# Kernel optimization log

Measured on AMD Instinct MI355X. Metric: run time of the kernel, lower is better.

The kernel has to match this reference:

```python
import jax, jax.numpy as jnp
import numpy as np

B, D, H, N, M, S = 64, 256, 512, 16384, 64, 3
EPS = 1e-4


def setup_inputs() -> dict:
    key = jax.random.key(0)
    ks = jax.random.split(key, 20)
    rn = lambda k, shape, sc=1.0: jax.random.normal(k, shape, dtype=jnp.float32) * sc
    z = lambda n: jnp.zeros((n,), jnp.float32)
    sc = 0.05
    return {
        "inp": rn(ks[0], (B, D)),
        "h_tm1": rn(ks[1], (B, H), 0.1),
        "c_tm1": rn(ks[2], (B, H), 0.1),
        "read_tm1": jax.nn.softmax(rn(ks[3], (B, N)), axis=-1),
        "write_tm1": jax.nn.softmax(rn(ks[4], (B, N)), axis=-1),
        "memory": rn(ks[5], (B, N, M), 0.1),
        "W_ih": rn(ks[6], (4 * H, D + M), sc), "b_ih": z(4 * H),
        "W_hh": rn(ks[7], (4 * H, H), sc), "b_hh": z(4 * H),
        "W_rk": rn(ks[8], (M, H), sc), "b_rk": z(M),
        "W_wk": rn(ks[9], (M, H), sc), "b_wk": z(M),
        "W_rc": rn(ks[10], (3, H), sc), "b_rc": z(3),
        "W_wc": rn(ks[11], (3, H), sc), "b_wc": z(3),
        "W_rs": rn(ks[12], (S, H), sc), "b_rs": z(S),
        "W_ws": rn(ks[13], (S, H), sc), "b_ws": z(S),
        "W_w": rn(ks[14], (2 * M, H), sc), "b_w": z(2 * M),
    }


def _head_params(h, Wk, bk, Wc, bc, Ws, bs):
    k = jnp.tanh(h @ Wk.T + bk)                 # [B, M] key
    c = h @ Wc.T + bc                           # [B, 3] beta/g/gamma raw
    s = jax.nn.softmax(h @ Ws.T + bs, axis=-1)  # [B, S] shift dist
    beta = jax.nn.relu(c[:, 0:1]) + EPS
    g = jax.nn.sigmoid(c[:, 1:2])
    gamma = jax.nn.relu(c[:, 2:3]) + 1.0 + EPS
    return k, s, beta, g, gamma


def _address(memory, w_tm1, k, s, beta, g, gamma):
    # content addressing: beta-scaled cosine similarity, softmax over slots
    dot = jnp.einsum('bm,bnm->bn', k, memory)                    # [B, N]
    nM = jnp.sqrt(jnp.sum(memory * memory, axis=-1)) + EPS       # [B, N]
    nk = jnp.sqrt(jnp.sum(k * k, axis=-1, keepdims=True)) + EPS  # [B, 1]
    content = jax.nn.softmax(beta * dot / (nM * nk), axis=-1)
    # interpolation with previous head
    inter = g * content + (1.0 - g) * w_tm1                      # [B, N]
    # circular shift conv: out[j] = sum_r s[r] * inter[(j + r - (S-1)) mod N]
    shifted = jnp.stack([jnp.roll(inter, S - 1 - r, axis=1) for r in range(S)], axis=-1)  # [B, N, S]
    conv = jnp.einsum('bns,bs->bn', shifted, s)
    # sharpening
    sharp = jnp.maximum(conv, 1e-8) ** gamma
    return sharp / jnp.sum(sharp, axis=1, keepdims=True)


def reference(inp, h_tm1, c_tm1, read_tm1, write_tm1, memory,
              W_ih, b_ih, W_hh, b_hh, W_rk, b_rk, W_wk, b_wk,
              W_rc, b_rc, W_wc, b_wc, W_rs, b_rs, W_ws, b_ws, W_w, b_w):
    # read head addressed from previous hidden state
    rk, rs, rbeta, rg, rgamma = _head_params(h_tm1, W_rk, b_rk, W_rc, b_rc, W_rs, b_rs)
    read_head = _address(memory, read_tm1, rk, rs, rbeta, rg, rgamma)
    M_read = jnp.einsum('bn,bnm->bm', read_head, memory)         # [B, M]
    # LSTMCell controller (torch gate order i, f, g, o)
    x = jnp.concatenate([inp, M_read], axis=1)
    gates = x @ W_ih.T + b_ih + h_tm1 @ W_hh.T + b_hh
    i, f, gg, o = jnp.split(gates, 4, axis=1)
    c_t = jax.nn.sigmoid(f) * c_tm1 + jax.nn.sigmoid(i) * jnp.tanh(gg)
    h_t = jax.nn.sigmoid(o) * jnp.tanh(c_t)
    # write head addressed from new hidden state
    wk, ws, wbeta, wg, wgamma = _head_params(h_t, W_wk, b_wk, W_wc, b_wc, W_ws, b_ws)
    write_head = _address(memory, write_tm1, wk, ws, wbeta, wg, wgamma)
    wa = h_t @ W_w.T + b_w
    e = jax.nn.sigmoid(wa[:, :M])                                # erase [B, M]
    a = wa[:, M:]                                                # add   [B, M]
    ww = write_head[:, :, None]                                  # [B, N, 1]
    M_out = memory * (1.0 - ww * e[:, None, :]) + ww * a[:, None, :]
    return (h_t, c_t, read_head, write_head, M_out)
```

## Files before the change

### kernel.cpp

```cpp
#include <hip/hip_runtime.h>
#include <hip/hip_bf16.h>
#include <math.h>

#define B_  64
#define D_  256
#define H_  512
#define N_  16384
#define M_  64
#define S_  3
#define EPS_ 1e-4f

__device__ __forceinline__ float sigmoidf_(float x) { return 1.0f / (1.0f + expf(-x)); }

template <bool WITH_W>
__global__ __launch_bounds__(256) void head_params_kernel(
    const float* __restrict__ h,
    const float* __restrict__ Wk, const float* __restrict__ bk,
    const float* __restrict__ Wc, const float* __restrict__ bc,
    const float* __restrict__ Ws, const float* __restrict__ bs,
    const float* __restrict__ Ww, const float* __restrict__ bw,
    float* __restrict__ k_out, float* __restrict__ nk_out,
    float* __restrict__ s_out,
    float* __restrict__ beta_out, float* __restrict__ g_out, float* __restrict__ gamma_out,
    float* __restrict__ e_out, float* __restrict__ a_out)
{
    const int b = blockIdx.x;
    const int tid = threadIdx.x;
    const int lane = tid & 63;
    const int wid = tid >> 6;
    __shared__ float raw[198];

    float h8[8];
    #pragma unroll
    for (int j = 0; j < 8; ++j) h8[j] = h[b * H_ + lane + 64 * j];

    const int count = WITH_W ? 198 : 70;
    for (int r = wid; r < count; r += 4) {
        const float* wrow;
        float bias;
        if (r < 64)       { wrow = Wk + r * H_;        bias = bk[r]; }
        else if (r < 67)  { wrow = Wc + (r - 64) * H_; bias = bc[r - 64]; }
        else if (r < 70)  { wrow = Ws + (r - 67) * H_; bias = bs[r - 67]; }
        else              { wrow = Ww + (r - 70) * H_; bias = bw[r - 70]; }
        float acc = 0.f;
        #pragma unroll
        for (int j = 0; j < 8; ++j) acc += wrow[lane + 64 * j] * h8[j];
        for (int off = 32; off >= 1; off >>= 1) acc += __shfl_xor(acc, off);
        if (lane == 0) raw[r] = acc + bias;
    }
    __syncthreads();

    if (tid < 64) {
        float kv = tanhf(raw[tid]);
        k_out[b * 64 + tid] = kv;
        float sq = kv * kv;
        for (int off = 32; off >= 1; off >>= 1) sq += __shfl_xor(sq, off);
        if (tid == 0) nk_out[b] = sqrtf(sq) + EPS_;
    } else if (tid == 64) {
        float c0 = raw[64], c1 = raw[65], c2 = raw[66];
        beta_out[b]  = fmaxf(c0, 0.f) + EPS_;
        g_out[b]     = sigmoidf_(c1);
        gamma_out[b] = fmaxf(c2, 0.f) + 1.f + EPS_;
    } else if (tid == 65) {
        float s0 = raw[67], s1 = raw[68], s2 = raw[69];
        float mx = fmaxf(s0, fmaxf(s1, s2));
        float e0 = expf(s0 - mx), e1 = expf(s1 - mx), e2 = expf(s2 - mx);
        float inv = 1.f / (e0 + e1 + e2);
        s_out[b * 3 + 0] = e0 * inv;
        s_out[b * 3 + 1] = e1 * inv;
        s_out[b * 3 + 2] = e2 * inv;
    }
    if (WITH_W && tid >= 128 && tid < 192) {
        int m = tid - 128;
        e_out[b * 64 + m] = sigmoidf_(raw[70 + m]);
        a_out[b * 64 + m] = raw[134 + m];
    }
}

template <bool COMPUTE_NM>
__global__ __launch_bounds__(256) void dot_kernel(
    const float* __restrict__ memory,
    const float* __restrict__ k,
    float* __restrict__ dot,
    float* __restrict__ nM)
{
    const int tid = threadIdx.x;
    const int lane = tid & 63;
    const int wid = tid >> 6;
    const int grp = lane >> 4;
    const int m16 = lane & 15;
    const int b = blockIdx.x >> 8;
    const int nbase = (blockIdx.x & 255) * 64;
    const float4 k4 = ((const float4*)(k + b * 64))[m16];
    const int slot = wid * 4 + grp;
    const size_t bbase = (size_t)b * N_;
    #pragma unroll
    for (int it = 0; it < 4; ++it) {
        const int n = nbase + it * 16 + slot;
        const float4 m4 = ((const float4*)(memory + (bbase + n) * 64))[m16];
        float d  = m4.x * k4.x + m4.y * k4.y + m4.z * k4.z + m4.w * k4.w;
        float sq = m4.x * m4.x + m4.y * m4.y + m4.z * m4.z + m4.w * m4.w;
        for (int off = 8; off >= 1; off >>= 1) {
            d += __shfl_xor(d, off);
            if (COMPUTE_NM) sq += __shfl_xor(sq, off);
        }
        if (m16 == 0) {
            dot[bbase + n] = d;
            if (COMPUTE_NM) nM[bbase + n] = sqrtf(sq) + EPS_;
        }
    }
}

__global__ __launch_bounds__(1024) void address_kernel(
    const float* __restrict__ dot,
    const float* __restrict__ nM,
    const float* __restrict__ w_tm1,
    const float* __restrict__ nk_a,
    const float* __restrict__ beta_a, const float* __restrict__ g_a,
    const float* __restrict__ gamma_a, const float* __restrict__ s_a,
    float* __restrict__ head_out)
{
    __shared__ float lds[N_];
    const int tid = threadIdx.x;
    const int b = blockIdx.x;
    const size_t base = (size_t)b * N_;
    const float beta = beta_a[b], g = g_a[b], gamma = gamma_a[b], nk = nk_a[b];
    const float s0 = s_a[b * 3 + 0], s1 = s_a[b * 3 + 1], s2 = s_a[b * 3 + 2];

    float lg[16];
    float lmax = -1e30f;
    #pragma unroll
    for (int t = 0; t < 16; ++t) {
        const int n = t * 1024 + tid;
        const float x = beta * dot[base + n] / (nM[base + n] * nk);
        lg[t] = x;
        lmax = fmaxf(lmax, x);
    }
    for (int off = 32; off >= 1; off >>= 1) lmax = fmaxf(lmax, __shfl_xor(lmax, off));
    if ((tid & 63) == 0) lds[tid >> 6] = lmax;
    __syncthreads();
    if (tid == 0) {
        float v = lds[0];
        for (int i = 1; i < 16; ++i) v = fmaxf(v, lds[i]);
        lds[16] = v;
    }
    __syncthreads();
    const float gmax = lds[16];

    float lsum = 0.f;
    #pragma unroll
    for (int t = 0; t < 16; ++t) { lg[t] = expf(lg[t] - gmax); lsum += lg[t]; }
    for (int off = 32; off >= 1; off >>= 1) lsum += __shfl_xor(lsum, off);
    if ((tid & 63) == 0) lds[tid >> 6] = lsum;
    __syncthreads();
    if (tid == 0) {
        float v = 0.f;
        for (int i = 0; i < 16; ++i) v += lds[i];
        lds[16] = v;
    }
    __syncthreads();
    const float inv_sum = 1.f / lds[16];
    __syncthreads();

    #pragma unroll
    for (int t = 0; t < 16; ++t) {
        const int n = t * 1024 + tid;
        lds[n] = g * lg[t] * inv_sum + (1.f - g) * w_tm1[base + n];
    }
    __syncthreads();

    float sh[16];
    float lsum2 = 0.f;
    #pragma unroll
    for (int t = 0; t < 16; ++t) {
        const int n = t * 1024 + tid;
        const float conv = s2 * lds[n] + s1 * lds[(n + N_ - 1) & (N_ - 1)]
                         + s0 * lds[(n + N_ - 2) & (N_ - 1)];
        const float v = powf(fmaxf(conv, 1e-8f), gamma);
        sh[t] = v;
        lsum2 += v;
    }
    __syncthreads();
    for (int off = 32; off >= 1; off >>= 1) lsum2 += __shfl_xor(lsum2, off);
    if ((tid & 63) == 0) lds[tid >> 6] = lsum2;
    __syncthreads();
    if (tid == 0) {
        float v = 0.f;
        for (int i = 0; i < 16; ++i) v += lds[i];
        lds[16] = v;
    }
    __syncthreads();
    const float inv2 = 1.f / lds[16];
    #pragma unroll
    for (int t = 0; t < 16; ++t) head_out[base + t * 1024 + tid] = sh[t] * inv2;
}

__global__ __launch_bounds__(256) void m_read_kernel(
    const float* __restrict__ memory,
    const float* __restrict__ head,
    float* __restrict__ M_read)
{
    const int tid = threadIdx.x;
    const int lane = tid & 63;
    const int wid = tid >> 6;
    const int grp = lane >> 4;
    const int m16 = lane & 15;
    const int b = blockIdx.x >> 6;
    const int nbase = (blockIdx.x & 63) * 256;
    const int slot = wid * 4 + grp;
    const size_t bbase = (size_t)b * N_;
    float4 acc = make_float4(0.f, 0.f, 0.f, 0.f);
    #pragma unroll 4
    for (int it = 0; it < 16; ++it) {
        const int n = nbase + it * 16 + slot;
        const float w = head[bbase + n];
        const float4 m4 = ((const float4*)(memory + (bbase + n) * 64))[m16];
        acc.x += w * m4.x; acc.y += w * m4.y; acc.z += w * m4.z; acc.w += w * m4.w;
    }
    for (int off = 32; off >= 16; off >>= 1) {
        acc.x += __shfl_xor(acc.x, off);
        acc.y += __shfl_xor(acc.y, off);
        acc.z += __shfl_xor(acc.z, off);
        acc.w += __shfl_xor(acc.w, off);
    }
    __shared__ float4 part[64];
    if (lane < 16) part[wid * 16 + lane] = acc;
    __syncthreads();
    if (tid < 16) {
        float4 t = part[tid];
        for (int w = 1; w < 4; ++w) {
            const float4 p = part[w * 16 + tid];
            t.x += p.x; t.y += p.y; t.z += p.z; t.w += p.w;
        }
        atomicAdd(&M_read[b * 64 + tid * 4 + 0], t.x);
        atomicAdd(&M_read[b * 64 + tid * 4 + 1], t.y);
        atomicAdd(&M_read[b * 64 + tid * 4 + 2], t.z);
        atomicAdd(&M_read[b * 64 + tid * 4 + 3], t.w);
    }
}

__global__ __launch_bounds__(256) void gates_splitk_kernel(
    const float* __restrict__ inp,
    const float* __restrict__ M_read,
    const float* __restrict__ h_tm1,
    const float* __restrict__ W_ih,
    const float* __restrict__ W_hh,
    float* __restrict__ gates)
{
    __shared__ __align__(16) float Xsm[64][68];
    __shared__ __align__(16) float Wsm[64][68];
    const int tid = threadIdx.x;
    const int jb = blockIdx.x & 31;
    const int c  = blockIdx.x >> 5;
    const int j0 = jb * 64;

    #pragma unroll
    for (int i = 0; i < 4; ++i) {
        const int e = i * 256 + tid;
        const int row = e >> 4;
        const int c4 = e & 15;
        const float* xrow;
        if (c < 4)       xrow = inp    + row * 256 + c * 64;
        else if (c == 4) xrow = M_read + row * 64;
        else             xrow = h_tm1  + row * 512 + (c - 5) * 64;
        const float4 v = ((const float4*)xrow)[c4];
        const int kl = c4 * 4;
        Xsm[kl + 0][row] = v.x; Xsm[kl + 1][row] = v.y;
        Xsm[kl + 2][row] = v.z; Xsm[kl + 3][row] = v.w;
    }
    #pragma unroll
    for (int i = 0; i < 4; ++i) {
        const int e = i * 256 + tid;
        const int row = e >> 4;
        const int c4 = e & 15;
        const float* wrow;
        if (c < 5) wrow = W_ih + (j0 + row) * 320 + c * 64;
        else       wrow = W_hh + (j0 + row) * 512 + (c - 5) * 64;
        const float4 v = ((const float4*)wrow)[c4];
        const int kl = c4 * 4;
        Wsm[kl + 0][row] = v.x; Wsm[kl + 1][row] = v.y;
        Wsm[kl + 2][row] = v.z; Wsm[kl + 3][row] = v.w;
    }
    __syncthreads();

    const int tx = tid & 15, ty = tid >> 4;
    float acc[4][4] = {};
    #pragma unroll
    for (int k = 0; k < 64; ++k) {
        const float4 av = *((const float4*)&Xsm[k][ty * 4]);
        const float4 wv = *((const float4*)&Wsm[k][tx * 4]);
        acc[0][0] += av.x * wv.x; acc[0][1] += av.x * wv.y; acc[0][2] += av.x * wv.z; acc[0][3] += av.x * wv.w;
        acc[1][0] += av.y * wv.x; acc[1][1] += av.y * wv.y; acc[1][2] += av.y * wv.z; acc[1][3] += av.y * wv.w;
        acc[2][0] += av.z * wv.x; acc[2][1] += av.z * wv.y; acc[2][2] += av.z * wv.z; acc[2][3] += av.z * wv.w;
        acc[3][0] += av.w * wv.x; acc[3][1] += av.w * wv.y; acc[3][2] += av.w * wv.z; acc[3][3] += av.w * wv.w;
    }
    #pragma unroll
    for (int bi = 0; bi < 4; ++bi) {
        const int b = ty * 4 + bi;
        #pragma unroll
        for (int ji = 0; ji < 4; ++ji) {
            atomicAdd(&gates[b * 2048 + j0 + tx * 4 + ji], acc[bi][ji]);
        }
    }
}

__global__ __launch_bounds__(256) void lstm_kernel(
    const float* __restrict__ gates,
    const float* __restrict__ b_ih, const float* __restrict__ b_hh,
    const float* __restrict__ c_tm1,
    float* __restrict__ h_out, float* __restrict__ c_out)
{
    const int idx = blockIdx.x * 256 + threadIdx.x;
    const int b = idx >> 9, j = idx & 511;
    const float* gr = gates + b * 2048;
    const float i_ = sigmoidf_(gr[j]        + b_ih[j]        + b_hh[j]);
    const float f_ = sigmoidf_(gr[512 + j]  + b_ih[512 + j]  + b_hh[512 + j]);
    const float g_ = tanhf(   gr[1024 + j] + b_ih[1024 + j] + b_hh[1024 + j]);
    const float o_ = sigmoidf_(gr[1536 + j] + b_ih[1536 + j] + b_hh[1536 + j]);
    const float c = f_ * c_tm1[idx] + i_ * g_;
    c_out[idx] = c;
    h_out[idx] = o_ * tanhf(c);
}

__global__ __launch_bounds__(256) void m_out_kernel(
    const float* __restrict__ memory,
    const float* __restrict__ whead,
    const float* __restrict__ e,
    const float* __restrict__ a,
    float* __restrict__ M_out)
{
    const size_t total = (size_t)B_ * N_ * 16;
    const size_t stride = (size_t)gridDim.x * 256;
    for (size_t idx = (size_t)blockIdx.x * 256 + threadIdx.x; idx < total; idx += stride) {
        const size_t nlin = idx >> 4;
        const int m4 = (int)(idx & 15);
        const int b = (int)(nlin >> 14);
        const float w = whead[nlin];
        const float4 ev = ((const float4*)(e + b * 64))[m4];
        const float4 av = ((const float4*)(a + b * 64))[m4];
        const float4 mv = ((const float4*)memory)[idx];
        float4 o;
        o.x = mv.x * (1.f - w * ev.x) + w * av.x;
        o.y = mv.y * (1.f - w * ev.y) + w * av.y;
        o.z = mv.z * (1.f - w * ev.z) + w * av.z;
        o.w = mv.w * (1.f - w * ev.w) + w * av.w;
        ((float4*)M_out)[idx] = o;
    }
}

extern "C" void kernel_launch(void* const* d_in, const int* in_sizes, int n_in,
                              void* d_out, int out_size, void* d_ws, size_t ws_size,
                              hipStream_t stream)
{
    const float* inp       = (const float*)d_in[0];
    const float* h_tm1     = (const float*)d_in[1];
    const float* c_tm1     = (const float*)d_in[2];
    const float* read_tm1  = (const float*)d_in[3];
    const float* write_tm1 = (const float*)d_in[4];
    const float* memory    = (const float*)d_in[5];
    const float* W_ih = (const float*)d_in[6];  const float* b_ih = (const float*)d_in[7];
    const float* W_hh = (const float*)d_in[8];  const float* b_hh = (const float*)d_in[9];
    const float* W_rk = (const float*)d_in[10]; const float* b_rk = (const float*)d_in[11];
    const float* W_wk = (const float*)d_in[12]; const float* b_wk = (const float*)d_in[13];
    const float* W_rc = (const float*)d_in[14]; const float* b_rc = (const float*)d_in[15];
    const float* W_wc = (const float*)d_in[16]; const float* b_wc = (const float*)d_in[17];
    const float* W_rs = (const float*)d_in[18]; const float* b_rs = (const float*)d_in[19];
    const float* W_ws = (const float*)d_in[20]; const float* b_ws = (const float*)d_in[21];
    const float* W_w  = (const float*)d_in[22]; const float* b_w  = (const float*)d_in[23];

    float* out = (float*)d_out;
    float* h_out   = out;
    float* c_out   = out + 32768;
    float* rhead   = out + 65536;
    float* whead   = out + 65536 + 1048576;
    float* Mout    = out + 65536 + 2 * 1048576;

    float* dot_r = rhead;
    float* dot_w = whead;
    float* nM    = Mout;

    float* ws = (float*)d_ws;
    float* gates  = ws;
    float* rk     = ws + 131072;
    float* wk     = ws + 135168;
    float* M_read = ws + 139264;
    float* e_buf  = ws + 143360;
    float* a_buf  = ws + 147456;
    float* rs     = ws + 151552;
    float* wss    = ws + 151744;
    float* rbeta  = ws + 151936;
    float* rg     = ws + 152000;
    float* rgamma = ws + 152064;
    float* rnk    = ws + 152128;
    float* wbeta  = ws + 152192;
    float* wg     = ws + 152256;
    float* wgamma = ws + 152320;
    float* wnk    = ws + 152384;

    hipMemsetAsync(M_read, 0, B_ * M_ * sizeof(float), stream);
    hipMemsetAsync(gates, 0, B_ * 4 * H_ * sizeof(float), stream);

    head_params_kernel<false><<<B_, 256, 0, stream>>>(
        h_tm1, W_rk, b_rk, W_rc, b_rc, W_rs, b_rs, nullptr, nullptr,
        rk, rnk, rs, rbeta, rg, rgamma, nullptr, nullptr);
    dot_kernel<true><<<B_ * 256, 256, 0, stream>>>(memory, rk, dot_r, nM);
    address_kernel<<<B_, 1024, 0, stream>>>(dot_r, nM, read_tm1, rnk, rbeta, rg, rgamma, rs, rhead);
    m_read_kernel<<<B_ * 64, 256, 0, stream>>>(memory, rhead, M_read);
    gates_splitk_kernel<<<13 * 32, 256, 0, stream>>>(inp, M_read, h_tm1, W_ih, W_hh, gates);
    lstm_kernel<<<128, 256, 0, stream>>>(gates, b_ih, b_hh, c_tm1, h_out, c_out);
    head_params_kernel<true><<<B_, 256, 0, stream>>>(
        h_out, W_wk, b_wk, W_wc, b_wc, W_ws, b_ws, W_w, b_w,
        wk, wnk, wss, wbeta, wg, wgamma, e_buf, a_buf);
    dot_kernel<false><<<B_ * 256, 256, 0, stream>>>(memory, wk, dot_w, nullptr);
    address_kernel<<<B_, 1024, 0, stream>>>(dot_w, nM, write_tm1, wnk, wbeta, wg, wgamma, wss, whead);
    m_out_kernel<<<16384, 256, 0, stream>>>(memory, whead, e_buf, a_buf, Mout);
}
```

Baseline: 781.7 us.

## Fuse entire NTM step into one cooperative persistent kernel with grid syncs

```diff
diff --git a/kernel.cpp b/kernel.cpp
--- a/kernel.cpp
+++ b/kernel.cpp
@@ -1,47 +1,101 @@
 #include <hip/hip_runtime.h>
-#include <hip/hip_bf16.h>
+#include <hip/hip_cooperative_groups.h>
 #include <math.h>
+
+namespace cg = cooperative_groups;
 
 #define B_  64
 #define D_  256
 #define H_  512
 #define N_  16384
 #define M_  64
-#define S_  3
 #define EPS_ 1e-4f
 
+#define NBLK 256
+#define NTHR 512
+#define CHUNK (N_ / 4)
+
+struct Args {
+  const float *inp, *h_tm1, *c_tm1, *read_tm1, *write_tm1, *memory;
+  const float *W_ih, *b_ih, *W_hh, *b_hh;
+  const float *W_rk, *b_rk, *W_wk, *b_wk;
+  const float *W_rc, *b_rc, *W_wc, *b_wc;
+  const float *W_rs, *b_rs, *W_ws, *b_ws;
+  const float *W_w, *b_w;
+  float *h_out, *c_out, *rhead, *whead, *Mout;
+  float *gates, *rk, *wk, *M_read, *e_buf, *a_buf, *rs, *wss;
+  float *rbeta, *rg, *rgamma, *rnk, *wbeta, *wg, *wgamma, *wnk;
+  float *Pmax, *Psum, *Psum2;
+};
+
+union Smem {
+  float raw[256];
+  float red[16];
+  float4 part4[128];
+  float cvinter[CHUNK + 2];
+  struct { float X[64][68]; float W[64][132]; } g;
+};
+
 __device__ __forceinline__ float sigmoidf_(float x) { return 1.0f / (1.0f + expf(-x)); }
 
-template <bool WITH_W>
-__global__ __launch_bounds__(256) void head_params_kernel(
-    const float* __restrict__ h,
-    const float* __restrict__ Wk, const float* __restrict__ bk,
-    const float* __restrict__ Wc, const float* __restrict__ bc,
-    const float* __restrict__ Ws, const float* __restrict__ bs,
-    const float* __restrict__ Ww, const float* __restrict__ bw,
-    float* __restrict__ k_out, float* __restrict__ nk_out,
-    float* __restrict__ s_out,
-    float* __restrict__ beta_out, float* __restrict__ g_out, float* __restrict__ gamma_out,
-    float* __restrict__ e_out, float* __restrict__ a_out)
+__device__ __forceinline__ void block_sum_to(float v, float* red, float* out) {
+    for (int off = 32; off >= 1; off >>= 1) v += __shfl_xor(v, off);
+    const int wid = threadIdx.x >> 6;
+    if ((threadIdx.x & 63) == 0) red[wid] = v;
+    __syncthreads();
+    if (threadIdx.x == 0) {
+        float s = red[0];
+        #pragma unroll
+        for (int i = 1; i < 8; ++i) s += red[i];
+        *out = s;
+    }
+    __syncthreads();
+}
+
+__device__ __forceinline__ void block_pair_to(float m, float s, float* red,
+                                              float* outm, float* outs) {
+    for (int off = 32; off >= 1; off >>= 1) {
+        float m2 = __shfl_xor(m, off), s2 = __shfl_xor(s, off);
+        float mn = fmaxf(m, m2);
+        s = s * expf(m - mn) + s2 * expf(m2 - mn);
+        m = mn;
+    }
+    const int wid = threadIdx.x >> 6;
+    if ((threadIdx.x & 63) == 0) { red[wid] = m; red[8 + wid] = s; }
+    __syncthreads();
+    if (threadIdx.x == 0) {
+        float M = red[0], S = red[8];
+        for (int i = 1; i < 8; ++i) {
+            float mn = fmaxf(M, red[i]);
+            S = S * expf(M - mn) + red[8 + i] * expf(red[i] - mn);
+            M = mn;
+        }
+        *outm = M; *outs = S;
+    }
+    __syncthreads();
+}
+
+__device__ void head_params(const float* h,
+    const float* Wk, const float* bk, const float* Wc, const float* bc,
+    const float* Ws, const float* bs, const float* Ww, const float* bw,
+    int with_w, int b,
+    float* k_out, float* nk_out, float* s_out,
+    float* beta_out, float* g_out, float* gamma_out,
+    float* e_out, float* a_out, float* raw)
 {
-    const int b = blockIdx.x;
     const int tid = threadIdx.x;
     const int lane = tid & 63;
     const int wid = tid >> 6;
-    __shared__ float raw[198];
-
     float h8[8];
     #pragma unroll
     for (int j = 0; j < 8; ++j) h8[j] = h[b * H_ + lane + 64 * j];
-
-    const int count = WITH_W ? 198 : 70;
-    for (int r = wid; r < count; r += 4) {
-        const float* wrow;
-        float bias;
-        if (r < 64)       { wrow = Wk + r * H_;        bias = bk[r]; }
-        else if (r < 67)  { wrow = Wc + (r - 64) * H_; bias = bc[r - 64]; }
-        else if (r < 70)  { wrow = Ws + (r - 67) * H_; bias = bs[r - 67]; }
-        else              { wrow = Ww + (r - 70) * H_; bias = bw[r - 70]; }
+    const int count = with_w ? 198 : 70;
+    for (int r = wid; r < count; r += 8) {
+        const float* wrow; float bias;
+        if (r < 64)      { wrow = Wk + r * H_;          bias = bk[r]; }
+        else if (r < 67) { wrow = Wc + (r - 64) * H_;   bias = bc[r - 64]; }
+        else if (r < 70) { wrow = Ws + (r - 67) * H_;   bias = bs[r - 67]; }
+        else             { wrow = Ww + (r - 70) * H_;   bias = bw[r - 70]; }
         float acc = 0.f;
         #pragma unroll
         for (int j = 0; j < 8; ++j) acc += wrow[lane + 64 * j] * h8[j];
@@ -49,7 +103,6 @@
         if (lane == 0) raw[r] = acc + bias;
     }
     __syncthreads();
-
     if (tid < 64) {
         float kv = tanhf(raw[tid]);
         k_out[b * 64 + tid] = kv;
@@ -57,10 +110,9 @@
         for (int off = 32; off >= 1; off >>= 1) sq += __shfl_xor(sq, off);
         if (tid == 0) nk_out[b] = sqrtf(sq) + EPS_;
     } else if (tid == 64) {
-        float c0 = raw[64], c1 = raw[65], c2 = raw[66];
-        beta_out[b]  = fmaxf(c0, 0.f) + EPS_;
-        g_out[b]     = sigmoidf_(c1);
-        gamma_out[b] = fmaxf(c2, 0.f) + 1.f + EPS_;
+        beta_out[b]  = fmaxf(raw[64], 0.f) + EPS_;
+        g_out[b]     = sigmoidf_(raw[65]);
+        gamma_out[b] = fmaxf(raw[66], 0.f) + 1.f + EPS_;
     } else if (tid == 65) {
         float s0 = raw[67], s1 = raw[68], s2 = raw[69];
         float mx = fmaxf(s0, fmaxf(s1, s2));
@@ -70,281 +122,295 @@
         s_out[b * 3 + 1] = e1 * inv;
         s_out[b * 3 + 2] = e2 * inv;
     }
-    if (WITH_W && tid >= 128 && tid < 192) {
+    if (with_w && tid >= 128 && tid < 192) {
         int m = tid - 128;
         e_out[b * 64 + m] = sigmoidf_(raw[70 + m]);
         a_out[b * 64 + m] = raw[134 + m];
     }
+    __syncthreads();
 }
 
-template <bool COMPUTE_NM>
-__global__ __launch_bounds__(256) void dot_kernel(
-    const float* __restrict__ memory,
-    const float* __restrict__ k,
-    float* __restrict__ dot,
-    float* __restrict__ nM)
+__global__ __launch_bounds__(NTHR) void ntm_mega(Args p)
 {
-    const int tid = threadIdx.x;
-    const int lane = tid & 63;
-    const int wid = tid >> 6;
-    const int grp = lane >> 4;
-    const int m16 = lane & 15;
-    const int b = blockIdx.x >> 8;
-    const int nbase = (blockIdx.x & 255) * 64;
-    const float4 k4 = ((const float4*)(k + b * 64))[m16];
-    const int slot = wid * 4 + grp;
+    cg::grid_group grid = cg::this_grid();
+    __shared__ Smem sm;
+
+    const int blk  = blockIdx.x;
+    const int tid  = threadIdx.x;
+    const int m16  = tid & 15;
+    const int rgrp = tid >> 4;
+    const int b    = blk >> 2;
+    const int cc   = blk & 3;
+    const int n0   = cc * CHUNK;
     const size_t bbase = (size_t)b * N_;
-    #pragma unroll
-    for (int it = 0; it < 4; ++it) {
-        const int n = nbase + it * 16 + slot;
-        const float4 m4 = ((const float4*)(memory + (bbase + n) * 64))[m16];
-        float d  = m4.x * k4.x + m4.y * k4.y + m4.z * k4.z + m4.w * k4.w;
-        float sq = m4.x * m4.x + m4.y * m4.y + m4.z * m4.z + m4.w * m4.w;
-        for (int off = 8; off >= 1; off >>= 1) {
-            d += __shfl_xor(d, off);
-            if (COMPUTE_NM) sq += __shfl_xor(sq, off);
-        }
-        if (m16 == 0) {
-            dot[bbase + n] = d;
-            if (COMPUTE_NM) nM[bbase + n] = sqrtf(sq) + EPS_;
-        }
-    }
-}
-
-__global__ __launch_bounds__(1024) void address_kernel(
-    const float* __restrict__ dot,
-    const float* __restrict__ nM,
-    const float* __restrict__ w_tm1,
-    const float* __restrict__ nk_a,
-    const float* __restrict__ beta_a, const float* __restrict__ g_a,
-    const float* __restrict__ gamma_a, const float* __restrict__ s_a,
-    float* __restrict__ head_out)
-{
-    __shared__ float lds[N_];
-    const int tid = threadIdx.x;
-    const int b = blockIdx.x;
-    const size_t base = (size_t)b * N_;
-    const float beta = beta_a[b], g = g_a[b], gamma = gamma_a[b], nk = nk_a[b];
-    const float s0 = s_a[b * 3 + 0], s1 = s_a[b * 3 + 1], s2 = s_a[b * 3 + 2];
-
-    float lg[16];
-    float lmax = -1e30f;
-    #pragma unroll
-    for (int t = 0; t < 16; ++t) {
-        const int n = t * 1024 + tid;
-        const float x = beta * dot[base + n] / (nM[base + n] * nk);
-        lg[t] = x;
-        lmax = fmaxf(lmax, x);
-    }
-    for (int off = 32; off >= 1; off >>= 1) lmax = fmaxf(lmax, __shfl_xor(lmax, off));
-    if ((tid & 63) == 0) lds[tid >> 6] = lmax;
-    __syncthreads();
-    if (tid == 0) {
-        float v = lds[0];
-        for (int i = 1; i < 16; ++i) v = fmaxf(v, lds[i]);
-        lds[16] = v;
-    }
-    __syncthreads();
-    const float gmax = lds[16];
-
-    float lsum = 0.f;
-    #pragma unroll
-    for (int t = 0; t < 16; ++t) { lg[t] = expf(lg[t] - gmax); lsum += lg[t]; }
-    for (int off = 32; off >= 1; off >>= 1) lsum += __shfl_xor(lsum, off);
-    if ((tid & 63) == 0) lds[tid >> 6] = lsum;
-    __syncthreads();
-    if (tid == 0) {
-        float v = 0.f;
-        for (int i = 0; i < 16; ++i) v += lds[i];
-        lds[16] = v;
-    }
-    __syncthreads();
-    const float inv_sum = 1.f / lds[16];
-    __syncthreads();
-
-    #pragma unroll
-    for (int t = 0; t < 16; ++t) {
-        const int n = t * 1024 + tid;
-        lds[n] = g * lg[t] * inv_sum + (1.f - g) * w_tm1[base + n];
-    }
-    __syncthreads();
-
-    float sh[16];
-    float lsum2 = 0.f;
-    #pragma unroll
-    for (int t = 0; t < 16; ++t) {
-        const int n = t * 1024 + tid;
-        const float conv = s2 * lds[n] + s1 * lds[(n + N_ - 1) & (N_ - 1)]
-                         + s0 * lds[(n + N_ - 2) & (N_ - 1)];
-        const float v = powf(fmaxf(conv, 1e-8f), gamma);
-        sh[t] = v;
-        lsum2 += v;
-    }
-    __syncthreads();
-    for (int off = 32; off >= 1; off >>= 1) lsum2 += __shfl_xor(lsum2, off);
-    if ((tid & 63) == 0) lds[tid >> 6] = lsum2;
-    __syncthreads();
-    if (tid == 0) {
-        float v = 0.f;
-        for (int i = 0; i < 16; ++i) v += lds[i];
-        lds[16] = v;
-    }
-    __syncthreads();
-    const float inv2 = 1.f / lds[16];
-    #pragma unroll
-    for (int t = 0; t < 16; ++t) head_out[base + t * 1024 + tid] = sh[t] * inv2;
-}
-
-__global__ __launch_bounds__(256) void m_read_kernel(
-    const float* __restrict__ memory,
-    const float* __restrict__ head,
-    float* __restrict__ M_read)
-{
-    const int tid = threadIdx.x;
-    const int lane = tid & 63;
-    const int wid = tid >> 6;
-    const int grp = lane >> 4;
-    const int m16 = lane & 15;
-    const int b = blockIdx.x >> 6;
-    const int nbase = (blockIdx.x & 63) * 256;
-    const int slot = wid * 4 + grp;
-    const size_t bbase = (size_t)b * N_;
-    float4 acc = make_float4(0.f, 0.f, 0.f, 0.f);
-    #pragma unroll 4
-    for (int it = 0; it < 16; ++it) {
-        const int n = nbase + it * 16 + slot;
-        const float w = head[bbase + n];
-        const float4 m4 = ((const float4*)(memory + (bbase + n) * 64))[m16];
-        acc.x += w * m4.x; acc.y += w * m4.y; acc.z += w * m4.z; acc.w += w * m4.w;
-    }
-    for (int off = 32; off >= 16; off >>= 1) {
-        acc.x += __shfl_xor(acc.x, off);
-        acc.y += __shfl_xor(acc.y, off);
-        acc.z += __shfl_xor(acc.z, off);
-        acc.w += __shfl_xor(acc.w, off);
-    }
-    __shared__ float4 part[64];
-    if (lane < 16) part[wid * 16 + lane] = acc;
-    __syncthreads();
-    if (tid < 16) {
-        float4 t = part[tid];
-        for (int w = 1; w < 4; ++w) {
-            const float4 p = part[w * 16 + tid];
-            t.x += p.x; t.y += p.y; t.z += p.z; t.w += p.w;
-        }
-        atomicAdd(&M_read[b * 64 + tid * 4 + 0], t.x);
-        atomicAdd(&M_read[b * 64 + tid * 4 + 1], t.y);
-        atomicAdd(&M_read[b * 64 + tid * 4 + 2], t.z);
-        atomicAdd(&M_read[b * 64 + tid * 4 + 3], t.w);
-    }
-}
-
-__global__ __launch_bounds__(256) void gates_splitk_kernel(
-    const float* __restrict__ inp,
-    const float* __restrict__ M_read,
-    const float* __restrict__ h_tm1,
-    const float* __restrict__ W_ih,
-    const float* __restrict__ W_hh,
-    float* __restrict__ gates)
-{
-    __shared__ __align__(16) float Xsm[64][68];
-    __shared__ __align__(16) float Wsm[64][68];
-    const int tid = threadIdx.x;
-    const int jb = blockIdx.x & 31;
-    const int c  = blockIdx.x >> 5;
-    const int j0 = jb * 64;
-
-    #pragma unroll
-    for (int i = 0; i < 4; ++i) {
-        const int e = i * 256 + tid;
-        const int row = e >> 4;
-        const int c4 = e & 15;
-        const float* xrow;
-        if (c < 4)       xrow = inp    + row * 256 + c * 64;
-        else if (c == 4) xrow = M_read + row * 64;
-        else             xrow = h_tm1  + row * 512 + (c - 5) * 64;
-        const float4 v = ((const float4*)xrow)[c4];
-        const int kl = c4 * 4;
-        Xsm[kl + 0][row] = v.x; Xsm[kl + 1][row] = v.y;
-        Xsm[kl + 2][row] = v.z; Xsm[kl + 3][row] = v.w;
-    }
-    #pragma unroll
-    for (int i = 0; i < 4; ++i) {
-        const int e = i * 256 + tid;
-        const int row = e >> 4;
-        const int c4 = e & 15;
-        const float* wrow;
-        if (c < 5) wrow = W_ih + (j0 + row) * 320 + c * 64;
-        else       wrow = W_hh + (j0 + row) * 512 + (c - 5) * 64;
-        const float4 v = ((const float4*)wrow)[c4];
-        const int kl = c4 * 4;
-        Wsm[kl + 0][row] = v.x; Wsm[kl + 1][row] = v.y;
-        Wsm[kl + 2][row] = v.z; Wsm[kl + 3][row] = v.w;
-    }
-    __syncthreads();
-
-    const int tx = tid & 15, ty = tid >> 4;
-    float acc[4][4] = {};
-    #pragma unroll
-    for (int k = 0; k < 64; ++k) {
-        const float4 av = *((const float4*)&Xsm[k][ty * 4]);
-        const float4 wv = *((const float4*)&Wsm[k][tx * 4]);
-        acc[0][0] += av.x * wv.x; acc[0][1] += av.x * wv.y; acc[0][2] += av.x * wv.z; acc[0][3] += av.x * wv.w;
-        acc[1][0] += av.y * wv.x; acc[1][1] += av.y * wv.y; acc[1][2] += av.y * wv.z; acc[1][3] += av.y * wv.w;
-        acc[2][0] += av.z * wv.x; acc[2][1] += av.z * wv.y; acc[2][2] += av.z * wv.z; acc[2][3] += av.z * wv.w;
-        acc[3][0] += av.w * wv.x; acc[3][1] += av.w * wv.y; acc[3][2] += av.w * wv.z; acc[3][3] += av.w * wv.w;
-    }
-    #pragma unroll
-    for (int bi = 0; bi < 4; ++bi) {
-        const int b = ty * 4 + bi;
-        #pragma unroll
-        for (int ji = 0; ji < 4; ++ji) {
-            atomicAdd(&gates[b * 2048 + j0 + tx * 4 + ji], acc[bi][ji]);
-        }
-    }
-}
-
-__global__ __launch_bounds__(256) void lstm_kernel(
-    const float* __restrict__ gates,
-    const float* __restrict__ b_ih, const float* __restrict__ b_hh,
-    const float* __restrict__ c_tm1,
-    float* __restrict__ h_out, float* __restrict__ c_out)
-{
-    const int idx = blockIdx.x * 256 + threadIdx.x;
-    const int b = idx >> 9, j = idx & 511;
-    const float* gr = gates + b * 2048;
-    const float i_ = sigmoidf_(gr[j]        + b_ih[j]        + b_hh[j]);
-    const float f_ = sigmoidf_(gr[512 + j]  + b_ih[512 + j]  + b_hh[512 + j]);
-    const float g_ = tanhf(   gr[1024 + j] + b_ih[1024 + j] + b_hh[1024 + j]);
-    const float o_ = sigmoidf_(gr[1536 + j] + b_ih[1536 + j] + b_hh[1536 + j]);
-    const float c = f_ * c_tm1[idx] + i_ * g_;
-    c_out[idx] = c;
-    h_out[idx] = o_ * tanhf(c);
-}
-
-__global__ __launch_bounds__(256) void m_out_kernel(
-    const float* __restrict__ memory,
-    const float* __restrict__ whead,
-    const float* __restrict__ e,
-    const float* __restrict__ a,
-    float* __restrict__ M_out)
-{
-    const size_t total = (size_t)B_ * N_ * 16;
-    const size_t stride = (size_t)gridDim.x * 256;
-    for (size_t idx = (size_t)blockIdx.x * 256 + threadIdx.x; idx < total; idx += stride) {
-        const size_t nlin = idx >> 4;
-        const int m4 = (int)(idx & 15);
-        const int b = (int)(nlin >> 14);
-        const float w = whead[nlin];
-        const float4 ev = ((const float4*)(e + b * 64))[m4];
-        const float4 av = ((const float4*)(a + b * 64))[m4];
-        const float4 mv = ((const float4*)memory)[idx];
-        float4 o;
-        o.x = mv.x * (1.f - w * ev.x) + w * av.x;
-        o.y = mv.y * (1.f - w * ev.y) + w * av.y;
-        o.z = mv.z * (1.f - w * ev.z) + w * av.z;
-        o.w = mv.w * (1.f - w * ev.w) + w * av.w;
-        ((float4*)M_out)[idx] = o;
+
+    float* xbuf  = p.Mout + (size_t)B_ * N_;
+    float* nMbuf = p.Mout;
+
+    if (blk < 64) {
+        head_params(p.h_tm1, p.W_rk, p.b_rk, p.W_rc, p.b_rc, p.W_rs, p.b_rs,
+                    nullptr, nullptr, 0, blk,
+                    p.rk, p.rnk, p.rs, p.rbeta, p.rg, p.rgamma, nullptr, nullptr, sm.raw);
+    } else {
+        for (int i = (blk - 64) * NTHR + tid; i < B_ * 4 * H_; i += 192 * NTHR)
+            p.gates[i] = 0.f;
+        if (blk == 64)
+            for (int i = tid; i < B_ * M_; i += NTHR) p.M_read[i] = 0.f;
+    }
+    grid.sync();
+
+    {
+        const float4 k4  = ((const float4*)(p.rk + b * 64))[m16];
+        const float beta = p.rbeta[b], nk = p.rnk[b];
+        float lm = -1e30f, ls = 0.f;
+        #pragma unroll 4
+        for (int it = 0; it < CHUNK / 32; ++it) {
+            const int n = n0 + it * 32 + rgrp;
+            const float4 m4 = ((const float4*)(p.memory + (bbase + n) * 64))[m16];
+            float d  = m4.x * k4.x + m4.y * k4.y + m4.z * k4.z + m4.w * k4.w;
+            float sq = m4.x * m4.x + m4.y * m4.y + m4.z * m4.z + m4.w * m4.w;
+            for (int off = 8; off >= 1; off >>= 1) {
+                d += __shfl_xor(d, off); sq += __shfl_xor(sq, off);
+            }
+            if (m16 == 0) {
+                float nMv = sqrtf(sq) + EPS_;
+                float x = beta * d / (nMv * nk);
+                xbuf[bbase + n]  = x;
+                nMbuf[bbase + n] = nMv;
+                float mn = fmaxf(lm, x);
+                ls = ls * expf(lm - mn) + expf(x - mn);
+                lm = mn;
+            }
+        }
+        block_pair_to(lm, ls, sm.red, &p.Pmax[blk], &p.Psum[blk]);
+    }
+    grid.sync();
+
+    {
+        float Mx = -1e30f, Sx = 0.f;
+        #pragma unroll
+        for (int c2 = 0; c2 < 4; ++c2) {
+            float m = p.Pmax[b * 4 + c2], s = p.Psum[b * 4 + c2];
+            float mn = fmaxf(Mx, m);
+            Sx = Sx * expf(Mx - mn) + s * expf(m - mn);
+            Mx = mn;
+        }
+        const float inv = 1.f / Sx, gmax = Mx;
+        const float g = p.rg[b], gamma = p.rgamma[b];
+        const float s0 = p.rs[b * 3 + 0], s1 = p.rs[b * 3 + 1], s2 = p.rs[b * 3 + 2];
+        #pragma unroll
+        for (int j = 0; j < CHUNK / NTHR; ++j) {
+            const int i = j * NTHR + tid;
+            const int n = n0 + i;
+            sm.cvinter[i + 2] = g * expf(xbuf[bbase + n] - gmax) * inv
+                              + (1.f - g) * p.read_tm1[bbase + n];
+        }
+        if (tid < 2) {
+            const int n = (n0 + N_ - 2 + tid) & (N_ - 1);
+            sm.cvinter[tid] = g * expf(xbuf[bbase + n] - gmax) * inv
+                            + (1.f - g) * p.read_tm1[bbase + n];
+        }
+        __syncthreads();
+        float lsum = 0.f;
+        #pragma unroll
+        for (int j = 0; j < CHUNK / NTHR; ++j) {
+            const int i = j * NTHR + tid;
+            const float conv = s2 * sm.cvinter[i + 2] + s1 * sm.cvinter[i + 1]
+                             + s0 * sm.cvinter[i];
+            const float v = powf(fmaxf(conv, 1e-8f), gamma);
+            p.whead[bbase + n0 + i] = v;
+            lsum += v;
+        }
+        __syncthreads();
+        block_sum_to(lsum, sm.red, &p.Psum2[blk]);
+    }
+    grid.sync();
+
+    {
+        const float inv2 = 1.f / (p.Psum2[b * 4 + 0] + p.Psum2[b * 4 + 1]
+                                + p.Psum2[b * 4 + 2] + p.Psum2[b * 4 + 3]);
+        float4 acc = make_float4(0.f, 0.f, 0.f, 0.f);
+        #pragma unroll 4
+        for (int it = 0; it < CHUNK / 32; ++it) {
+            const int n = n0 + it * 32 + rgrp;
+            const float w = p.whead[bbase + n] * inv2;
+            const float4 m4 = ((const float4*)(p.memory + (bbase + n) * 64))[m16];
+            if (m16 == 0) p.rhead[bbase + n] = w;
+            acc.x += w * m4.x; acc.y += w * m4.y; acc.z += w * m4.z; acc.w += w * m4.w;
+        }
+        for (int off = 16; off <= 32; off <<= 1) {
+            acc.x += __shfl_xor(acc.x, off); acc.y += __shfl_xor(acc.y, off);
+            acc.z += __shfl_xor(acc.z, off); acc.w += __shfl_xor(acc.w, off);
+        }
+        const int lane = tid & 63, wid = tid >> 6;
+        if (lane < 16) sm.part4[wid * 16 + lane] = acc;
+        __syncthreads();
+        if (tid < 16) {
+            float4 t = sm.part4[tid];
+            for (int w2 = 1; w2 < 8; ++w2) {
+                const float4 q = sm.part4[w2 * 16 + tid];
+                t.x += q.x; t.y += q.y; t.z += q.z; t.w += q.w;
+            }
+            atomicAdd(&p.M_read[b * 64 + tid * 4 + 0], t.x);
+            atomicAdd(&p.M_read[b * 64 + tid * 4 + 1], t.y);
+            atomicAdd(&p.M_read[b * 64 + tid * 4 + 2], t.z);
+            atomicAdd(&p.M_read[b * 64 + tid * 4 + 3], t.w);
+        }
+        __syncthreads();
+    }
+    grid.sync();
+
+    if (blk < 208) {
+        const int jt = blk & 15;
+        const int ch = blk >> 4;
+        const int j0 = jt * 128;
+        #pragma unroll
+        for (int i = 0; i < 2; ++i) {
+            const int e = i * NTHR + tid;
+            const int row = e >> 4, c4 = e & 15;
+            const float* xrow;
+            if (ch < 4)       xrow = p.inp    + row * 256 + ch * 64;
+            else if (ch == 4) xrow = p.M_read + row * 64;
+            else              xrow = p.h_tm1  + row * 512 + (ch - 5) * 64;
+            const float4 v = ((const float4*)xrow)[c4];
+            const int kl = c4 * 4;
+            sm.g.X[kl + 0][row] = v.x; sm.g.X[kl + 1][row] = v.y;
+            sm.g.X[kl + 2][row] = v.z; sm.g.X[kl + 3][row] = v.w;
+        }
+        #pragma unroll
+        for (int i = 0; i < 4; ++i) {
+            const int e = i * NTHR + tid;
+            const int row = e >> 4, c4 = e & 15;
+            const float* wrow;
+            if (ch < 5) wrow = p.W_ih + (size_t)(j0 + row) * 320 + ch * 64;
+            else        wrow = p.W_hh + (size_t)(j0 + row) * 512 + (ch - 5) * 64;
+            const float4 v = ((const float4*)wrow)[c4];
+            const int kl = c4 * 4;
+            sm.g.W[kl + 0][row] = v.x; sm.g.W[kl + 1][row] = v.y;
+            sm.g.W[kl + 2][row] = v.z; sm.g.W[kl + 3][row] = v.w;
+        }
+        __syncthreads();
+        const int tx = tid & 31, ty = tid >> 5;
+        float acc2[4][4] = {};
+        #pragma unroll
+        for (int k = 0; k < 64; ++k) {
+            const float4 av = *((const float4*)&sm.g.X[k][ty * 4]);
+            const float4 wv = *((const float4*)&sm.g.W[k][tx * 4]);
+            acc2[0][0] += av.x * wv.x; acc2[0][1] += av.x * wv.y; acc2[0][2] += av.x * wv.z; acc2[0][3] += av.x * wv.w;
+            acc2[1][0] += av.y * wv.x; acc2[1][1] += av.y * wv.y; acc2[1][2] += av.y * wv.z; acc2[1][3] += av.y * wv.w;
+            acc2[2][0] += av.z * wv.x; acc2[2][1] += av.z * wv.y; acc2[2][2] += av.z * wv.z; acc2[2][3] += av.z * wv.w;
+            acc2[3][0] += av.w * wv.x; acc2[3][1] += av.w * wv.y; acc2[3][2] += av.w * wv.z; acc2[3][3] += av.w * wv.w;
+        }
+        #pragma unroll
+        for (int bi = 0; bi < 4; ++bi)
+            #pragma unroll
+            for (int ji = 0; ji < 4; ++ji)
+                atomicAdd(&p.gates[(ty * 4 + bi) * 2048 + j0 + tx * 4 + ji], acc2[bi][ji]);
+        __syncthreads();
+    }
+    grid.sync();
+
+    if (tid < 128) {
+        const int idx = blk * 128 + tid;
+        const int bb = idx >> 9, j = idx & 511;
+        const float* gr = p.gates + bb * 2048;
+        const float i_ = sigmoidf_(gr[j]        + p.b_ih[j]        + p.b_hh[j]);
+        const float f_ = sigmoidf_(gr[512 + j]  + p.b_ih[512 + j]  + p.b_hh[512 + j]);
+        const float g_ = tanhf(   gr[1024 + j] + p.b_ih[1024 + j] + p.b_hh[1024 + j]);
+        const float o_ = sigmoidf_(gr[1536 + j] + p.b_ih[1536 + j] + p.b_hh[1536 + j]);
+        const float cv = f_ * p.c_tm1[idx] + i_ * g_;
+        p.c_out[idx] = cv;
+        p.h_out[idx] = o_ * tanhf(cv);
+    }
+    grid.sync();
+
+    if (blk < 64) {
+        head_params(p.h_out, p.W_wk, p.b_wk, p.W_wc, p.b_wc, p.W_ws, p.b_ws,
+                    p.W_w, p.b_w, 1, blk,
+                    p.wk, p.wnk, p.wss, p.wbeta, p.wg, p.wgamma, p.e_buf, p.a_buf, sm.raw);
+    }
+    grid.sync();
+
+    {
+        const float4 k4  = ((const float4*)(p.wk + b * 64))[m16];
+        const float beta = p.wbeta[b], nk = p.wnk[b];
+        float lm = -1e30f, ls = 0.f;
+        #pragma unroll 4
+        for (int it = 0; it < CHUNK / 32; ++it) {
+            const int n = n0 + it * 32 + rgrp;
+            const float4 m4 = ((const float4*)(p.memory + (bbase + n) * 64))[m16];
+            float d = m4.x * k4.x + m4.y * k4.y + m4.z * k4.z + m4.w * k4.w;
+            for (int off = 8; off >= 1; off >>= 1) d += __shfl_xor(d, off);
+            if (m16 == 0) {
+                float x = beta * d / (nMbuf[bbase + n] * nk);
+                xbuf[bbase + n] = x;
+                float mn = fmaxf(lm, x);
+                ls = ls * expf(lm - mn) + expf(x - mn);
+                lm = mn;
+            }
+        }
+        block_pair_to(lm, ls, sm.red, &p.Pmax[blk], &p.Psum[blk]);
+    }
+    grid.sync();
+
+    {
+        float Mx = -1e30f, Sx = 0.f;
+        #pragma unroll
+        for (int c2 = 0; c2 < 4; ++c2) {
+            float m = p.Pmax[b * 4 + c2], s = p.Psum[b * 4 + c2];
+            float mn = fmaxf(Mx, m);
+            Sx = Sx * expf(Mx - mn) + s * expf(m - mn);
+            Mx = mn;
+        }
+        const float inv = 1.f / Sx, gmax = Mx;
+        const float g = p.wg[b], gamma = p.wgamma[b];
+        const float s0 = p.wss[b * 3 + 0], s1 = p.wss[b * 3 + 1], s2 = p.wss[b * 3 + 2];
+        #pragma unroll
+        for (int j = 0; j < CHUNK / NTHR; ++j) {
+            const int i = j * NTHR + tid;
+            const int n = n0 + i;
+            sm.cvinter[i + 2] = g * expf(xbuf[bbase + n] - gmax) * inv
+                              + (1.f - g) * p.write_tm1[bbase + n];
+        }
+        if (tid < 2) {
+            const int n = (n0 + N_ - 2 + tid) & (N_ - 1);
+            sm.cvinter[tid] = g * expf(xbuf[bbase + n] - gmax) * inv
+                            + (1.f - g) * p.write_tm1[bbase + n];
+        }
+        __syncthreads();
+        float lsum = 0.f;
+        #pragma unroll
+        for (int j = 0; j < CHUNK / NTHR; ++j) {
+            const int i = j * NTHR + tid;
+            const float conv = s2 * sm.cvinter[i + 2] + s1 * sm.cvinter[i + 1]
+                             + s0 * sm.cvinter[i];
+            const float v = powf(fmaxf(conv, 1e-8f), gamma);
+            p.whead[bbase + n0 + i] = v;
+            lsum += v;
+        }
+        __syncthreads();
+        block_sum_to(lsum, sm.red, &p.Psum2[blk]);
+    }
+    grid.sync();
+
+    {
+        const float inv2 = 1.f / (p.Psum2[b * 4 + 0] + p.Psum2[b * 4 + 1]
+                                + p.Psum2[b * 4 + 2] + p.Psum2[b * 4 + 3]);
+        const float4 e4 = ((const float4*)(p.e_buf + b * 64))[m16];
+        const float4 a4 = ((const float4*)(p.a_buf + b * 64))[m16];
+        #pragma unroll 4
+        for (int it = 0; it < CHUNK / 32; ++it) {
+            const int n = n0 + it * 32 + rgrp;
+            const float w = p.whead[bbase + n] * inv2;
+            const float4 m4 = ((const float4*)(p.memory + (bbase + n) * 64))[m16];
+            if (m16 == 0) p.whead[bbase + n] = w;
+            float4 o;
+            o.x = m4.x * (1.f - w * e4.x) + w * a4.x;
+            o.y = m4.y * (1.f - w * e4.y) + w * a4.y;
+            o.z = m4.z * (1.f - w * e4.z) + w * a4.z;
+            o.w = m4.w * (1.f - w * e4.w) + w * a4.w;
+            ((float4*)(p.Mout + (bbase + n) * 64))[m16] = o;
+        }
     }
 }
 
@@ -352,66 +418,52 @@
                               void* d_out, int out_size, void* d_ws, size_t ws_size,
                               hipStream_t stream)
 {
-    const float* inp       = (const float*)d_in[0];
-    const float* h_tm1     = (const float*)d_in[1];
-    const float* c_tm1     = (const float*)d_in[2];
-    const float* read_tm1  = (const float*)d_in[3];
-    const float* write_tm1 = (const float*)d_in[4];
-    const float* memory    = (const float*)d_in[5];
-    const float* W_ih = (const float*)d_in[6];  const float* b_ih = (const float*)d_in[7];
-    const float* W_hh = (const float*)d_in[8];  const float* b_hh = (const float*)d_in[9];
-    const float* W_rk = (const float*)d_in[10]; const float* b_rk = (const float*)d_in[11];
-    const float* W_wk = (const float*)d_in[12]; const float* b_wk = (const float*)d_in[13];
-    const float* W_rc = (const float*)d_in[14]; const float* b_rc = (const float*)d_in[15];
-    const float* W_wc = (const float*)d_in[16]; const float* b_wc = (const float*)d_in[17];
-    const float* W_rs = (const float*)d_in[18]; const float* b_rs = (const float*)d_in[19];
-    const float* W_ws = (const float*)d_in[20]; const float* b_ws = (const float*)d_in[21];
-    const float* W_w  = (const float*)d_in[22]; const float* b_w  = (const float*)d_in[23];
+    Args p;
+    p.inp       = (const float*)d_in[0];
+    p.h_tm1     = (const float*)d_in[1];
+    p.c_tm1     = (const float*)d_in[2];
+    p.read_tm1  = (const float*)d_in[3];
+    p.write_tm1 = (const float*)d_in[4];
+    p.memory    = (const float*)d_in[5];
+    p.W_ih = (const float*)d_in[6];  p.b_ih = (const float*)d_in[7];
+    p.W_hh = (const float*)d_in[8];  p.b_hh = (const float*)d_in[9];
+    p.W_rk = (const float*)d_in[10]; p.b_rk = (const float*)d_in[11];
+    p.W_wk = (const float*)d_in[12]; p.b_wk = (const float*)d_in[13];
+    p.W_rc = (const float*)d_in[14]; p.b_rc = (const float*)d_in[15];
+    p.W_wc = (const float*)d_in[16]; p.b_wc = (const float*)d_in[17];
+    p.W_rs = (const float*)d_in[18]; p.b_rs = (const float*)d_in[19];
+    p.W_ws = (const float*)d_in[20]; p.b_ws = (const float*)d_in[21];
+    p.W_w  = (const float*)d_in[22]; p.b_w  = (const float*)d_in[23];
 
     float* out = (float*)d_out;
-    float* h_out   = out;
-    float* c_out   = out + 32768;
-    float* rhead   = out + 65536;
-    float* whead   = out + 65536 + 1048576;
-    float* Mout    = out + 65536 + 2 * 1048576;
-
-    float* dot_r = rhead;
-    float* dot_w = whead;
-    float* nM    = Mout;
+    p.h_out = out;
+    p.c_out = out + 32768;
+    p.rhead = out + 65536;
+    p.whead = out + 65536 + 1048576;
+    p.Mout  = out + 65536 + 2 * 1048576;
 
     float* ws = (float*)d_ws;
-    float* gates  = ws;
-    float* rk     = ws + 131072;
-    float* wk     = ws + 135168;
-    float* M_read = ws + 139264;
-    float* e_buf  = ws + 143360;
-    float* a_buf  = ws + 147456;
-    float* rs     = ws + 151552;
-    float* wss    = ws + 151744;
-    float* rbeta  = ws + 151936;
-    float* rg     = ws + 152000;
-    float* rgamma = ws + 152064;
-    float* rnk    = ws + 152128;
-    float* wbeta  = ws + 152192;
-    float* wg     = ws + 152256;
-    float* wgamma = ws + 152320;
-    float* wnk    = ws + 152384;
-
-    hipMemsetAsync(M_read, 0, B_ * M_ * sizeof(float), stream);
-    hipMemsetAsync(gates, 0, B_ * 4 * H_ * sizeof(float), stream);
-
-    head_params_kernel<false><<<B_, 256, 0, stream>>>(
-        h_tm1, W_rk, b_rk, W_rc, b_rc, W_rs, b_rs, nullptr, nullptr,
-        rk, rnk, rs, rbeta, rg, rgamma, nullptr, nullptr);
-    dot_kernel<true><<<B_ * 256, 256, 0, stream>>>(memory, rk, dot_r, nM);
-    address_kernel<<<B_, 1024, 0, stream>>>(dot_r, nM, read_tm1, rnk, rbeta, rg, rgamma, rs, rhead);
-    m_read_kernel<<<B_ * 64, 256, 0, stream>>>(memory, rhead, M_read);
-    gates_splitk_kernel<<<13 * 32, 256, 0, stream>>>(inp, M_read, h_tm1, W_ih, W_hh, gates);
-    lstm_kernel<<<128, 256, 0, stream>>>(gates, b_ih, b_hh, c_tm1, h_out, c_out);
-    head_params_kernel<true><<<B_, 256, 0, stream>>>(
-        h_out, W_wk, b_wk, W_wc, b_wc, W_ws, b_ws, W_w, b_w,
-        wk, wnk, wss, wbeta, wg, wgamma, e_buf, a_buf);
-    dot_kernel<false><<<B_ * 256, 256, 0, stream>>>(memory, wk, dot_w, nullptr);
-    address_kernel<<<B_, 1024, 0, stream>>>(dot_w, nM, write_tm1, wnk, wbeta, wg, wgamma, wss, whead);
-    m_out_kernel<<<16384, 256, 0, stream>>>(memory, whead, e_buf, a_buf, Mout);
+    p.gates  = ws;
+    p.rk     = ws + 131072;
+    p.wk     = ws + 135168;
+    p.M_read = ws + 139264;
+    p.e_buf  = ws + 143360;
+    p.a_buf  = ws + 147456;
+    p.rs     = ws + 151552;
+    p.wss    = ws + 151744;
+    p.rbeta  = ws + 151936;
+    p.rg     = ws + 152000;
+    p.rgamma = ws + 152064;
+    p.rnk    = ws + 152128;
+    p.wbeta  = ws + 152192;
+    p.wg     = ws + 152256;
+    p.wgamma = ws + 152320;
+    p.wnk    = ws + 152384;
+    p.Pmax   = ws + 152448;
+    p.Psum   = ws + 152704;
+    p.Psum2  = ws + 152960;
+
+    void* kargs[] = { (void*)&p };
+    hipLaunchCooperativeKernel((const void*)ntm_mega, dim3(NBLK), dim3(NTHR),
+                               kargs, 0, stream);
 }
```

Measured after the change: 1.214 ms. 55.2% more time.
